# Kernel tuning notes

Hardware: AMD Instinct MI355X
Metric: run time of the kernel (lower is better)

Reference implementation:

```python
import jax, jax.numpy as jnp
import numpy as np

B, S, EMBED, FFN, NQ = 8, 2048, 1024, 4096, 8

def setup_inputs() -> dict:
    key = jax.random.key(0)
    ks = jax.random.split(key, 6)
    return {
        "x": jax.random.normal(ks[0], (B, S, EMBED), dtype=jnp.float32),
        "theta": jax.random.normal(ks[1], (NQ,), dtype=jnp.float32),
        "W1": jax.random.normal(ks[2], (FFN, NQ), dtype=jnp.float32) * (1.0 / np.sqrt(NQ)),
        "b1": jax.random.normal(ks[3], (FFN,), dtype=jnp.float32) * 0.02,
        "W2": jax.random.normal(ks[4], (EMBED, FFN), dtype=jnp.float32) * (1.0 / np.sqrt(FFN)),
        "b2": jax.random.normal(ks[5], (EMBED,), dtype=jnp.float32) * 0.02,
    }

def reference(x, theta, W1, b1, W2, b2):
    # Quantum layer (product circuit, closed form): per qubit i,
    # |0> -RX(x_i)-> -RY(theta_i)->, <PauliZ> = cos(x_i) * cos(theta_i).
    nq = theta.shape[0]
    q = jnp.cos(x[..., :nq]) * jnp.cos(theta)        # [B,S,NQ]
    # dropout is identity in eval mode
    h = jax.nn.relu(jnp.einsum('bsq,fq->bsf', q, W1) + b1)  # [B,S,FFN]
    return jnp.einsum('bsf,ef->bse', h, W2) + b2            # [B,S,EMBED]
```

## Files before the change

kernel.cpp:

```cpp
#include <hip/hip_runtime.h>
#include <cstdint>
#include <cstddef>

#define AS1 __attribute__((address_space(1)))
#define AS3 __attribute__((address_space(3)))

typedef __bf16 bf16x8 __attribute__((ext_vector_type(8)));
typedef float  f32x16 __attribute__((ext_vector_type(16)));

#define MDIM 16384
#define NDIM 1024
#define KDIM 4096
#define NQ   8

#define BM 128
#define BN 128
#define BK 64

__global__ __launch_bounds__(256) void conv_w2_kernel(const float* __restrict__ W2,
                                                      __bf16* __restrict__ W2b) {
    size_t base = ((size_t)blockIdx.x * 256 + threadIdx.x) * 8;
    float4 a = *(const float4*)(W2 + base);
    float4 b = *(const float4*)(W2 + base + 4);
    bf16x8 v;
    v[0] = (__bf16)a.x; v[1] = (__bf16)a.y; v[2] = (__bf16)a.z; v[3] = (__bf16)a.w;
    v[4] = (__bf16)b.x; v[5] = (__bf16)b.y; v[6] = (__bf16)b.z; v[7] = (__bf16)b.w;
    *(bf16x8*)(W2b + base) = v;
}

__global__ __launch_bounds__(256) void qh_kernel(const float* __restrict__ x,
                                                 const float* __restrict__ theta,
                                                 const float* __restrict__ W1,
                                                 const float* __restrict__ b1,
                                                 __bf16* __restrict__ H) {
    const int t  = threadIdx.x;
    const int m0 = blockIdx.x * 32;

    float ct[NQ];
#pragma unroll
    for (int i = 0; i < NQ; ++i) ct[i] = __cosf(theta[i]);

#pragma unroll 1
    for (int rc = 0; rc < 4; ++rc) {
        const int mbase = m0 + rc * 8;
        float q[8][NQ];
#pragma unroll
        for (int r = 0; r < 8; ++r) {
            const float4 xa = *(const float4*)(x + (size_t)(mbase + r) * 1024);
            const float4 xb = *(const float4*)(x + (size_t)(mbase + r) * 1024 + 4);
            q[r][0] = __cosf(xa.x) * ct[0];
            q[r][1] = __cosf(xa.y) * ct[1];
            q[r][2] = __cosf(xa.z) * ct[2];
            q[r][3] = __cosf(xa.w) * ct[3];
            q[r][4] = __cosf(xb.x) * ct[4];
            q[r][5] = __cosf(xb.y) * ct[5];
            q[r][6] = __cosf(xb.z) * ct[6];
            q[r][7] = __cosf(xb.w) * ct[7];
        }
#pragma unroll 1
        for (int j = 0; j < 16; ++j) {
            const int f = j * 256 + t;
            const float4 wa = *(const float4*)(W1 + (size_t)f * NQ);
            const float4 wb = *(const float4*)(W1 + (size_t)f * NQ + 4);
            const float bb = b1[f];
#pragma unroll
            for (int r = 0; r < 8; ++r) {
                float a = bb
                        + q[r][0] * wa.x + q[r][1] * wa.y + q[r][2] * wa.z + q[r][3] * wa.w
                        + q[r][4] * wb.x + q[r][5] * wb.y + q[r][6] * wb.z + q[r][7] * wb.w;
                a = a > 0.f ? a : 0.f;
                H[(size_t)(mbase + r) * KDIM + f] = (__bf16)a;
            }
        }
    }
}

__global__ __launch_bounds__(256) void gemm_bt_kernel(const __bf16* __restrict__ A,
                                                      const __bf16* __restrict__ B,
                                                      const float* __restrict__ bias,
                                                      float* __restrict__ C) {
    __shared__ __align__(16) __bf16 Al[BM * BK];
    __shared__ __align__(16) __bf16 Bl[BN * BK];

    const int tid  = threadIdx.x;
    const int wave = tid >> 6;
    const int lane = tid & 63;
    const int bm = blockIdx.x;
    const int bn = blockIdx.y;

    const int lr = lane >> 3;
    const int ul = (lane & 7) ^ lr;
    const size_t arow = (size_t)(bm * BM + wave * 32 + lr);
    const size_t brow = (size_t)(bn * BN + wave * 32 + lr);
    const __bf16* gA0 = A + arow * KDIM + ul * 8;
    const __bf16* gB0 = B + brow * KDIM + ul * 8;
    __bf16* lA0 = &Al[(wave * 32) * BK];
    __bf16* lB0 = &Bl[(wave * 32) * BK];

    const int fl = lane & 31;
    const int fq = lane >> 5;
    const int sw = fl & 7;
    const int ma[2] = { (wave & 1) * 64 + fl, (wave & 1) * 64 + 32 + fl };
    const int na[2] = { (wave >> 1) * 64 + fl, (wave >> 1) * 64 + 32 + fl };

    f32x16 acc[2][2] = {};

    for (int kt = 0; kt < KDIM; kt += BK) {
        __syncthreads();
#pragma unroll
        for (int c = 0; c < 4; ++c) {
            __builtin_amdgcn_global_load_lds((AS1 void*)(gA0 + (size_t)c * 8 * KDIM + kt),
                                             (AS3 void*)(lA0 + c * 8 * BK), 16, 0, 0);
            __builtin_amdgcn_global_load_lds((AS1 void*)(gB0 + (size_t)c * 8 * KDIM + kt),
                                             (AS3 void*)(lB0 + c * 8 * BK), 16, 0, 0);
        }
        __syncthreads();
#pragma unroll
        for (int t4 = 0; t4 < 4; ++t4) {
            bf16x8 af[2], bfr[2];
            const int u = (t4 * 2 + fq) ^ sw;
#pragma unroll
            for (int i = 0; i < 2; ++i) {
                af[i]  = *(const bf16x8*)&Al[ma[i] * BK + u * 8];
                bfr[i] = *(const bf16x8*)&Bl[na[i] * BK + u * 8];
            }
            acc[0][0] = __builtin_amdgcn_mfma_f32_32x32x16_bf16(af[0], bfr[0], acc[0][0], 0, 0, 0);
            acc[0][1] = __builtin_amdgcn_mfma_f32_32x32x16_bf16(af[0], bfr[1], acc[0][1], 0, 0, 0);
            acc[1][0] = __builtin_amdgcn_mfma_f32_32x32x16_bf16(af[1], bfr[0], acc[1][0], 0, 0, 0);
            acc[1][1] = __builtin_amdgcn_mfma_f32_32x32x16_bf16(af[1], bfr[1], acc[1][1], 0, 0, 0);
        }
    }

    const int cm0 = bm * BM + (wave & 1) * 64;
    const int cn0 = bn * BN + (wave >> 1) * 64;
#pragma unroll
    for (int i = 0; i < 2; ++i) {
#pragma unroll
        for (int j = 0; j < 2; ++j) {
            const int col = cn0 + j * 32 + fl;
            const float bv = bias[col];
#pragma unroll
            for (int r = 0; r < 16; ++r) {
                const int row = cm0 + i * 32 + (r & 3) + 8 * (r >> 2) + 4 * fq;
                C[(size_t)row * NDIM + col] = acc[i][j][r] + bv;
            }
        }
    }
}

extern "C" void kernel_launch(void* const* d_in, const int* in_sizes, int n_in,
                              void* d_out, int out_size, void* d_ws, size_t ws_size,
                              hipStream_t stream) {
    const float* x     = (const float*)d_in[0];
    const float* theta = (const float*)d_in[1];
    const float* W1    = (const float*)d_in[2];
    const float* b1    = (const float*)d_in[3];
    const float* W2    = (const float*)d_in[4];
    const float* b2    = (const float*)d_in[5];
    float* out = (float*)d_out;

    __bf16* H   = (__bf16*)d_ws;
    __bf16* W2b = (__bf16*)((char*)d_ws + (size_t)MDIM * KDIM * 2);

    conv_w2_kernel<<<(KDIM * NDIM) / (256 * 8), 256, 0, stream>>>(W2, W2b);
    qh_kernel<<<MDIM / 32, 256, 0, stream>>>(x, theta, W1, b1, H);
    gemm_bt_kernel<<<dim3(MDIM / BM, NDIM / BN), 256, 0, stream>>>(H, W2b, b2, out);
}
```

Measured before the change: 334.1 us.

## Enlarge GEMM tiles to 256x256 and restructure H generation for vector stores

The bf16 GEMM block tile grows from 128x128 to 256x256, and each wave now computes a 128x128 sub-tile with a 4x4 grid of MFMA accumulators. This raises reuse of the fragments loaded from LDS and halves global traffic per output, at the cost of many more registers, 64KB of LDS and a grid of only 256 blocks. The qh kernel is remapped so each thread keeps 8 W1 rows in registers and writes 8 consecutive bf16 H values with one vector store. This replaces the scattered scalar 2-byte stores.

```diff
diff --git a/kernel.cpp b/kernel.cpp
--- a/kernel.cpp
+++ b/kernel.cpp
@@ -13,8 +13,8 @@
 #define KDIM 4096
 #define NQ   8
 
-#define BM 128
-#define BN 128
+#define BM 256
+#define BN 256
 #define BK 64
 
 __global__ __launch_bounds__(256) void conv_w2_kernel(const float* __restrict__ W2,
@@ -28,57 +28,62 @@
     *(bf16x8*)(W2b + base) = v;
 }
 
+#define QROWS 64
 __global__ __launch_bounds__(256) void qh_kernel(const float* __restrict__ x,
                                                  const float* __restrict__ theta,
                                                  const float* __restrict__ W1,
                                                  const float* __restrict__ b1,
                                                  __bf16* __restrict__ H) {
     const int t  = threadIdx.x;
-    const int m0 = blockIdx.x * 32;
+    const int f0 = blockIdx.y * 2048 + t * 8;
+    const int r0 = blockIdx.x * QROWS;
 
+    float w[8][8];
+#pragma unroll
+    for (int fr = 0; fr < 8; ++fr) {
+        float4 a = *(const float4*)(W1 + (size_t)(f0 + fr) * NQ);
+        float4 b = *(const float4*)(W1 + (size_t)(f0 + fr) * NQ + 4);
+        w[fr][0] = a.x; w[fr][1] = a.y; w[fr][2] = a.z; w[fr][3] = a.w;
+        w[fr][4] = b.x; w[fr][5] = b.y; w[fr][6] = b.z; w[fr][7] = b.w;
+    }
+    float bias[8];
+    {
+        float4 a = *(const float4*)(b1 + f0);
+        float4 b = *(const float4*)(b1 + f0 + 4);
+        bias[0] = a.x; bias[1] = a.y; bias[2] = a.z; bias[3] = a.w;
+        bias[4] = b.x; bias[5] = b.y; bias[6] = b.z; bias[7] = b.w;
+    }
     float ct[NQ];
 #pragma unroll
     for (int i = 0; i < NQ; ++i) ct[i] = __cosf(theta[i]);
 
 #pragma unroll 1
-    for (int rc = 0; rc < 4; ++rc) {
-        const int mbase = m0 + rc * 8;
-        float q[8][NQ];
+    for (int r = 0; r < QROWS; ++r) {
+        const float* xr = x + (size_t)(r0 + r) * 1024;
+        const float4 xa = *(const float4*)xr;
+        const float4 xb = *(const float4*)(xr + 4);
+        float q[8];
+        q[0] = __cosf(xa.x) * ct[0]; q[1] = __cosf(xa.y) * ct[1];
+        q[2] = __cosf(xa.z) * ct[2]; q[3] = __cosf(xa.w) * ct[3];
+        q[4] = __cosf(xb.x) * ct[4]; q[5] = __cosf(xb.y) * ct[5];
+        q[6] = __cosf(xb.z) * ct[6]; q[7] = __cosf(xb.w) * ct[7];
+        bf16x8 o;
 #pragma unroll
-        for (int r = 0; r < 8; ++r) {
-            const float4 xa = *(const float4*)(x + (size_t)(mbase + r) * 1024);
-            const float4 xb = *(const float4*)(x + (size_t)(mbase + r) * 1024 + 4);
-            q[r][0] = __cosf(xa.x) * ct[0];
-            q[r][1] = __cosf(xa.y) * ct[1];
-            q[r][2] = __cosf(xa.z) * ct[2];
-            q[r][3] = __cosf(xa.w) * ct[3];
-            q[r][4] = __cosf(xb.x) * ct[4];
-            q[r][5] = __cosf(xb.y) * ct[5];
-            q[r][6] = __cosf(xb.z) * ct[6];
-            q[r][7] = __cosf(xb.w) * ct[7];
+        for (int fr = 0; fr < 8; ++fr) {
+            float a = bias[fr];
+#pragma unroll
+            for (int i = 0; i < 8; ++i) a += q[i] * w[fr][i];
+            a = fmaxf(a, 0.f);
+            o[fr] = (__bf16)a;
         }
-#pragma unroll 1
-        for (int j = 0; j < 16; ++j) {
-            const int f = j * 256 + t;
-            const float4 wa = *(const float4*)(W1 + (size_t)f * NQ);
-            const float4 wb = *(const float4*)(W1 + (size_t)f * NQ + 4);
-            const float bb = b1[f];
-#pragma unroll
-            for (int r = 0; r < 8; ++r) {
-                float a = bb
-                        + q[r][0] * wa.x + q[r][1] * wa.y + q[r][2] * wa.z + q[r][3] * wa.w
-                        + q[r][4] * wb.x + q[r][5] * wb.y + q[r][6] * wb.z + q[r][7] * wb.w;
-                a = a > 0.f ? a : 0.f;
-                H[(size_t)(mbase + r) * KDIM + f] = (__bf16)a;
-            }
-        }
+        *(bf16x8*)(H + (size_t)(r0 + r) * KDIM + f0) = o;
     }
 }
 
-__global__ __launch_bounds__(256) void gemm_bt_kernel(const __bf16* __restrict__ A,
-                                                      const __bf16* __restrict__ B,
-                                                      const float* __restrict__ bias,
-                                                      float* __restrict__ C) {
+__global__ __launch_bounds__(256, 1) void gemm_bt_kernel(const __bf16* __restrict__ A,
+                                                         const __bf16* __restrict__ B,
+                                                         const float* __restrict__ bias,
+                                                         float* __restrict__ C) {
     __shared__ __align__(16) __bf16 Al[BM * BK];
     __shared__ __align__(16) __bf16 Bl[BN * BK];
 
@@ -90,25 +95,23 @@
 
     const int lr = lane >> 3;
     const int ul = (lane & 7) ^ lr;
-    const size_t arow = (size_t)(bm * BM + wave * 32 + lr);
-    const size_t brow = (size_t)(bn * BN + wave * 32 + lr);
-    const __bf16* gA0 = A + arow * KDIM + ul * 8;
-    const __bf16* gB0 = B + brow * KDIM + ul * 8;
-    __bf16* lA0 = &Al[(wave * 32) * BK];
-    __bf16* lB0 = &Bl[(wave * 32) * BK];
+    const __bf16* gA0 = A + (size_t)(bm * BM + wave * 64 + lr) * KDIM + ul * 8;
+    const __bf16* gB0 = B + (size_t)(bn * BN + wave * 64 + lr) * KDIM + ul * 8;
+    __bf16* lA0 = &Al[(wave * 64) * BK];
+    __bf16* lB0 = &Bl[(wave * 64) * BK];
 
     const int fl = lane & 31;
     const int fq = lane >> 5;
     const int sw = fl & 7;
-    const int ma[2] = { (wave & 1) * 64 + fl, (wave & 1) * 64 + 32 + fl };
-    const int na[2] = { (wave >> 1) * 64 + fl, (wave >> 1) * 64 + 32 + fl };
+    const int wm = (wave & 1) * 128;
+    const int wn = (wave >> 1) * 128;
 
-    f32x16 acc[2][2] = {};
+    f32x16 acc[4][4] = {};
 
     for (int kt = 0; kt < KDIM; kt += BK) {
         __syncthreads();
 #pragma unroll
-        for (int c = 0; c < 4; ++c) {
+        for (int c = 0; c < 8; ++c) {
             __builtin_amdgcn_global_load_lds((AS1 void*)(gA0 + (size_t)c * 8 * KDIM + kt),
                                              (AS3 void*)(lA0 + c * 8 * BK), 16, 0, 0);
             __builtin_amdgcn_global_load_lds((AS1 void*)(gB0 + (size_t)c * 8 * KDIM + kt),
@@ -117,34 +120,34 @@
         __syncthreads();
 #pragma unroll
         for (int t4 = 0; t4 < 4; ++t4) {
-            bf16x8 af[2], bfr[2];
-            const int u = (t4 * 2 + fq) ^ sw;
+            const int u = ((t4 * 2 + fq) ^ sw) * 8;
+            bf16x8 af[4], bfr[4];
 #pragma unroll
-            for (int i = 0; i < 2; ++i) {
-                af[i]  = *(const bf16x8*)&Al[ma[i] * BK + u * 8];
-                bfr[i] = *(const bf16x8*)&Bl[na[i] * BK + u * 8];
+            for (int i = 0; i < 4; ++i) {
+                af[i]  = *(const bf16x8*)&Al[(wm + i * 32 + fl) * BK + u];
+                bfr[i] = *(const bf16x8*)&Bl[(wn + i * 32 + fl) * BK + u];
             }
-            acc[0][0] = __builtin_amdgcn_mfma_f32_32x32x16_bf16(af[0], bfr[0], acc[0][0], 0, 0, 0);
-            acc[0][1] = __builtin_amdgcn_mfma_f32_32x32x16_bf16(af[0], bfr[1], acc[0][1], 0, 0, 0);
-            acc[1][0] = __builtin_amdgcn_mfma_f32_32x32x16_bf16(af[1], bfr[0], acc[1][0], 0, 0, 0);
-            acc[1][1] = __builtin_amdgcn_mfma_f32_32x32x16_bf16(af[1], bfr[1], acc[1][1], 0, 0, 0);
+#pragma unroll
+            for (int i = 0; i < 4; ++i)
+#pragma unroll
+                for (int j = 0; j < 4; ++j)
+                    acc[i][j] = __builtin_amdgcn_mfma_f32_32x32x16_bf16(af[i], bfr[j], acc[i][j], 0, 0, 0);
         }
     }
 
-    const int cm0 = bm * BM + (wave & 1) * 64;
-    const int cn0 = bn * BN + (wave >> 1) * 64;
+    const int cm0 = bm * BM + wm;
+    const int cn0 = bn * BN + wn;
 #pragma unroll
-    for (int i = 0; i < 2; ++i) {
+    for (int j = 0; j < 4; ++j) {
+        const int col = cn0 + j * 32 + fl;
+        const float bv = bias[col];
 #pragma unroll
-        for (int j = 0; j < 2; ++j) {
-            const int col = cn0 + j * 32 + fl;
-            const float bv = bias[col];
+        for (int i = 0; i < 4; ++i)
 #pragma unroll
             for (int r = 0; r < 16; ++r) {
                 const int row = cm0 + i * 32 + (r & 3) + 8 * (r >> 2) + 4 * fq;
                 C[(size_t)row * NDIM + col] = acc[i][j][r] + bv;
             }
-        }
     }
 }
 
@@ -163,6 +166,6 @@
     __bf16* W2b = (__bf16*)((char*)d_ws + (size_t)MDIM * KDIM * 2);
 
     conv_w2_kernel<<<(KDIM * NDIM) / (256 * 8), 256, 0, stream>>>(W2, W2b);
-    qh_kernel<<<MDIM / 32, 256, 0, stream>>>(x, theta, W1, b1, H);
+    qh_kernel<<<dim3(MDIM / QROWS, KDIM / 2048), 256, 0, stream>>>(x, theta, W1, b1, H);
     gemm_bt_kernel<<<dim3(MDIM / BM, NDIM / BN), 256, 0, stream>>>(H, W2b, b2, out);
 }
```

Result: no change. 332.1 us (-0.6%).
